# Optimization experiments

Measured on AMD Instinct MI355X. Metric: run time of the kernel, lower is better.

## Reference

```python
import jax, jax.numpy as jnp
import numpy as np

INPUT_SIZE = 256
N_DIM = 128
BATCH = 1024


def setup_inputs() -> dict:
    key = jax.random.key(0)
    ks = jax.random.split(key, 8)
    X = jax.random.normal(ks[0], (BATCH, INPUT_SIZE), dtype=jnp.float32)
    h = jax.random.normal(ks[1], (BATCH, INPUT_SIZE * N_DIM), dtype=jnp.float32)
    W_r = jax.random.normal(ks[2], (INPUT_SIZE, 1, N_DIM), dtype=jnp.float32)
    W_z = jax.random.normal(ks[3], (INPUT_SIZE, 1, N_DIM), dtype=jnp.float32)
    W_h = jax.random.normal(ks[4], (INPUT_SIZE, 1, N_DIM), dtype=jnp.float32)
    # orthogonal init for U (matches nn.init.orthogonal_ in spirit)
    def ortho(k):
        a = jax.random.normal(k, (INPUT_SIZE, N_DIM, N_DIM), dtype=jnp.float32)
        q, _ = jnp.linalg.qr(a)
        return q.astype(jnp.float32)
    U_r = ortho(ks[5])
    U_z = ortho(ks[6])
    U_h = ortho(ks[7])
    b_r = jnp.zeros((INPUT_SIZE, N_DIM), dtype=jnp.float32)
    b_z = jnp.zeros((INPUT_SIZE, N_DIM), dtype=jnp.float32)
    b_h = jnp.zeros((INPUT_SIZE, N_DIM), dtype=jnp.float32)
    return {"X": X, "h": h, "W_r": W_r, "W_z": W_z, "W_h": W_h,
            "U_r": U_r, "U_z": U_z, "U_h": U_h,
            "b_r": b_r, "b_z": b_z, "b_h": b_h}


def reference(X, h, W_r, W_z, W_h, U_r, U_z, U_h, b_r, b_z, b_h):
    B = X.shape[0]
    hg = h.reshape(B, INPUT_SIZE, N_DIM)  # [B, I, D]
    # X contribution: X[b,i] * W[i,0,k] -> [B, I, D]
    xW_r = X[:, :, None] * W_r[:, 0, :][None]
    xW_z = X[:, :, None] * W_z[:, 0, :][None]
    xW_h = X[:, :, None] * W_h[:, 0, :][None]
    # grouped GEMMs: [B,I,D] x [I,D,D] -> [B,I,D]
    r = jax.nn.sigmoid(xW_r + jnp.einsum('bij,ijk->bik', hg, U_r) + b_r)
    z = jax.nn.sigmoid(xW_z + jnp.einsum('bij,ijk->bik', hg, U_z) + b_z)
    h_tilde = jnp.tanh(xW_h + jnp.einsum('bij,ijk->bik', r * hg, U_h) + b_h)
    h_new = z * hg + (1.0 - z) * h_tilde
    return (h_new.reshape(B, INPUT_SIZE * N_DIM),
            h_tilde.reshape(B, INPUT_SIZE * N_DIM))
```

## Files before the change

### kernel.cpp

```cpp
#include <hip/hip_runtime.h>
#include <hip/hip_bf16.h>
#include <stdint.h>

#define I_SIZE 256
#define D_DIM 128
#define BATCH 1024

typedef __attribute__((ext_vector_type(8))) short short8;
typedef __attribute__((ext_vector_type(4))) short short4v;
typedef __attribute__((ext_vector_type(4))) float floatx4;

__device__ inline short f2bf(float f) {
    union { float f; uint32_t u; } v; v.f = f;
    uint32_t u = v.u;
    uint32_t r = (u + 0x7FFFu + ((u >> 16) & 1u)) >> 16;
    return (short)(r & 0xFFFFu);
}
__device__ inline float bf2f(short s) {
    union { uint32_t u; float f; } v; v.u = ((uint32_t)(uint16_t)s) << 16;
    return v.f;
}
__device__ inline uint32_t pkbf(float a, float b) {
    __hip_bfloat162 h = __float22bfloat162_rn(make_float2(a, b));
    union { __hip_bfloat162 h; uint32_t u; } v; v.h = h; return v.u;
}
__device__ inline float sigmoidf_fast(float x) { return 1.0f / (1.0f + __expf(-x)); }
__device__ inline float tanhf_fast(float x)    { return 2.0f / (1.0f + __expf(-2.0f * x)) - 1.0f; }

#define BAR_LGKM() asm volatile("s_waitcnt lgkmcnt(0)\n\ts_barrier" ::: "memory")

#define S_H 136

__global__ __launch_bounds__(1024, 4) void gru_fused(
    const float* __restrict__ X, const float* __restrict__ H,
    const float* __restrict__ Wr, const float* __restrict__ Wz, const float* __restrict__ Wh,
    const float* __restrict__ Ur, const float* __restrict__ Uz, const float* __restrict__ Uh,
    const float* __restrict__ br, const float* __restrict__ bz, const float* __restrict__ bh,
    float* __restrict__ out)
{
    __shared__ short Ut[3 * D_DIM * D_DIM];
    __shared__ short hgb[D_DIM * S_H];
    __shared__ float Wl[6][D_DIM];
    __shared__ float Xl[BATCH];

    const int tid   = threadIdx.x;
    const int group = blockIdx.x;
    const int lane  = tid & 63;
    const int w     = tid >> 6;

    if (tid < D_DIM) {
        Wl[0][tid] = Wr[group * D_DIM + tid];
        Wl[1][tid] = Wz[group * D_DIM + tid];
        Wl[2][tid] = Wh[group * D_DIM + tid];
        Wl[3][tid] = br[group * D_DIM + tid];
        Wl[4][tid] = bz[group * D_DIM + tid];
        Wl[5][tid] = bh[group * D_DIM + tid];
    }
    Xl[tid] = X[(size_t)tid * I_SIZE + group];

    {
        const int kc = tid & 127;
        const int jb = tid >> 7;
        #pragma unroll
        for (int g = 0; g < 3; ++g) {
            const float* Ug = ((g == 0) ? Ur : (g == 1) ? Uz : Uh)
                              + (size_t)group * (D_DIM * D_DIM);
            short* dst = &Ut[g * (D_DIM * D_DIM)];
            #pragma unroll
            for (int m = 0; m < 4; ++m) {
                const int j0 = m * 8 + jb;
                float a0 = Ug[(4 * j0 + 0) * D_DIM + kc];
                float a1 = Ug[(4 * j0 + 1) * D_DIM + kc];
                float a2 = Ug[(4 * j0 + 2) * D_DIM + kc];
                float a3 = Ug[(4 * j0 + 3) * D_DIM + kc];
                short4v s; s.x = f2bf(a0); s.y = f2bf(a1); s.z = f2bf(a2); s.w = f2bf(a3);
                const int p = (j0 >> 1) ^ (kc & 7);
                *(short4v*)&dst[kc * D_DIM + p * 8 + 4 * (j0 & 1)] = s;
            }
        }
    }

    const int srow = tid >> 3;
    const int scol = (tid & 7) * 4;

    #pragma unroll
    for (int it = 0; it < 4; ++it) {
        int col = scol + it * 32;
        float4 v = *(const float4*)(H + (size_t)srow * (I_SIZE * D_DIM)
                                    + group * D_DIM + col);
        uint2 uu; uu.x = pkbf(v.x, v.y); uu.y = pkbf(v.z, v.w);
        *(uint2*)&hgb[srow * S_H + col] = uu;
    }
    BAR_LGKM();

    const int am = lane & 15;
    const int aq = lane >> 4;
    const int rg = w >> 1;
    const int nh = w & 1;
    const int r0 = rg * 16;
    const size_t HOFF = (size_t)BATCH * I_SIZE * D_DIM;

    int pswz[4];
    #pragma unroll
    for (int kk = 0; kk < 4; ++kk) pswz[kk] = ((4 * kk + aq) ^ (am & 7)) * 8;

    const floatx4 zero = {0.f, 0.f, 0.f, 0.f};

    for (int pass = 0; pass < 8; ++pass) {
        const int R = pass * 128;

        short8 a[4];
        #pragma unroll
        for (int kk = 0; kk < 4; ++kk)
            a[kk] = *(const short8*)&hgb[(r0 + am) * S_H + kk * 32 + aq * 8];

        float4 pf[4];
        if (pass < 7) {
            #pragma unroll
            for (int it = 0; it < 4; ++it) {
                int col = scol + it * 32;
                pf[it] = *(const float4*)(H + (size_t)(R + 128 + srow) * (I_SIZE * D_DIM)
                                          + group * D_DIM + col);
            }
        }

        floatx4 accr[4], accz[4];
        #pragma unroll
        for (int t2 = 0; t2 < 4; ++t2) { accr[t2] = zero; accz[t2] = zero; }

        #pragma unroll
        for (int t2 = 0; t2 < 4; ++t2) {
            const int n = nh * 64 + t2 * 16 + am;
            const short* rowp = &Ut[n * D_DIM];
            #pragma unroll
            for (int kk = 0; kk < 4; ++kk)
                accr[t2] = __builtin_amdgcn_mfma_f32_16x16x32_bf16(
                    a[kk], *(const short8*)(rowp + pswz[kk]), accr[t2], 0, 0, 0);
            #pragma unroll
            for (int kk = 0; kk < 4; ++kk)
                accz[t2] = __builtin_amdgcn_mfma_f32_16x16x32_bf16(
                    a[kk], *(const short8*)(rowp + 16384 + pswz[kk]), accz[t2], 0, 0, 0);
        }

        float Xv[4];
        #pragma unroll
        for (int pp = 0; pp < 4; ++pp)
            Xv[pp] = Xl[R + r0 + aq * 4 + pp];

        float zr[4][4], hgc[4][4];
        #pragma unroll
        for (int t2 = 0; t2 < 4; ++t2) {
            const int c = nh * 64 + t2 * 16 + am;
            const float wr = Wl[0][c], wz = Wl[1][c], brv = Wl[3][c], bzv = Wl[4][c];
            #pragma unroll
            for (int pp = 0; pp < 4; ++pp) {
                const int rl = r0 + aq * 4 + pp;
                float hgv = bf2f(hgb[rl * S_H + c]);
                float rv = sigmoidf_fast(accr[t2][pp] + Xv[pp] * wr + brv);
                float zv = sigmoidf_fast(accz[t2][pp] + Xv[pp] * wz + bzv);
                zr[t2][pp]  = zv;
                hgc[t2][pp] = hgv;
                hgb[rl * S_H + c] = f2bf(rv * hgv);
            }
        }
        BAR_LGKM();

        short8 ap[4];
        #pragma unroll
        for (int kk = 0; kk < 4; ++kk)
            ap[kk] = *(const short8*)&hgb[(r0 + am) * S_H + kk * 32 + aq * 8];

        floatx4 acch[4];
        #pragma unroll
        for (int t2 = 0; t2 < 4; ++t2) acch[t2] = zero;
        #pragma unroll
        for (int t2 = 0; t2 < 4; ++t2) {
            const int n = nh * 64 + t2 * 16 + am;
            const short* rowp = &Ut[32768 + n * D_DIM];
            #pragma unroll
            for (int kk = 0; kk < 4; ++kk)
                acch[t2] = __builtin_amdgcn_mfma_f32_16x16x32_bf16(
                    ap[kk], *(const short8*)(rowp + pswz[kk]), acch[t2], 0, 0, 0);
        }

        #pragma unroll
        for (int t2 = 0; t2 < 4; ++t2) {
            const int c = nh * 64 + t2 * 16 + am;
            const float wh = Wl[2][c], bhv = Wl[5][c];
            #pragma unroll
            for (int pp = 0; pp < 4; ++pp) {
                const int rl = r0 + aq * 4 + pp;
                float ht = tanhf_fast(acch[t2][pp] + Xv[pp] * wh + bhv);
                float zv = zr[t2][pp];
                float hn = zv * hgc[t2][pp] + (1.0f - zv) * ht;
                size_t o = (size_t)(R + rl) * (I_SIZE * D_DIM) + group * D_DIM + c;
                out[o]        = hn;
                out[HOFF + o] = ht;
            }
        }

        if (pass < 7) {
            BAR_LGKM();
            #pragma unroll
            for (int it = 0; it < 4; ++it) {
                int col = scol + it * 32;
                uint2 uu; uu.x = pkbf(pf[it].x, pf[it].y); uu.y = pkbf(pf[it].z, pf[it].w);
                *(uint2*)&hgb[srow * S_H + col] = uu;
            }
            BAR_LGKM();
        }
    }
}

extern "C" void kernel_launch(void* const* d_in, const int* in_sizes, int n_in,
                              void* d_out, int out_size, void* d_ws, size_t ws_size,
                              hipStream_t stream) {
    const float* X  = (const float*)d_in[0];
    const float* H  = (const float*)d_in[1];
    const float* Wr = (const float*)d_in[2];
    const float* Wz = (const float*)d_in[3];
    const float* Wh = (const float*)d_in[4];
    const float* Ur = (const float*)d_in[5];
    const float* Uz = (const float*)d_in[6];
    const float* Uh = (const float*)d_in[7];
    const float* br = (const float*)d_in[8];
    const float* bz = (const float*)d_in[9];
    const float* bh = (const float*)d_in[10];

    (void)d_ws; (void)ws_size;

    gru_fused<<<dim3(I_SIZE), dim3(1024), 0, stream>>>(
        X, H, Wr, Wz, Wh, Ur, Uz, Uh, br, bz, bh, (float*)d_out);
}
```

Baseline: 430.7 us.

## Compute full r-gate per wave to remove mid-pass barrier, swizzle h buffer

Each wave now computes the r-gate for all 128 output columns of its 16 rows, redundantly, instead of splitting columns across a wave pair. Because each wave fills its own rows of a separate r*h buffer, the block-wide barrier between the r/z phase and the h-tilde GEMM becomes a local lgkmcnt wait. The h buffer drops its padding in favour of an XOR swizzle, W/b/X move from LDS to registers and direct global loads, and MFMA sections get s_setprio. The trade is extra r-gate MFMA and sigmoid work and more register pressure.

```diff
diff --git a/kernel.cpp b/kernel.cpp
--- a/kernel.cpp
+++ b/kernel.cpp
@@ -7,15 +7,8 @@
 #define BATCH 1024
 
 typedef __attribute__((ext_vector_type(8))) short short8;
-typedef __attribute__((ext_vector_type(4))) short short4v;
 typedef __attribute__((ext_vector_type(4))) float floatx4;
 
-__device__ inline short f2bf(float f) {
-    union { float f; uint32_t u; } v; v.f = f;
-    uint32_t u = v.u;
-    uint32_t r = (u + 0x7FFFu + ((u >> 16) & 1u)) >> 16;
-    return (short)(r & 0xFFFFu);
-}
 __device__ inline float bf2f(short s) {
     union { uint32_t u; float f; } v; v.u = ((uint32_t)(uint16_t)s) << 16;
     return v.f;
@@ -28,8 +21,6 @@
 __device__ inline float tanhf_fast(float x)    { return 2.0f / (1.0f + __expf(-2.0f * x)) - 1.0f; }
 
 #define BAR_LGKM() asm volatile("s_waitcnt lgkmcnt(0)\n\ts_barrier" ::: "memory")
-
-#define S_H 136
 
 __global__ __launch_bounds__(1024, 4) void gru_fused(
     const float* __restrict__ X, const float* __restrict__ H,
@@ -39,24 +30,36 @@
     float* __restrict__ out)
 {
     __shared__ short Ut[3 * D_DIM * D_DIM];
-    __shared__ short hgb[D_DIM * S_H];
-    __shared__ float Wl[6][D_DIM];
-    __shared__ float Xl[BATCH];
+    __shared__ short hgb[D_DIM * D_DIM];
+    __shared__ short pb [D_DIM * D_DIM];
 
     const int tid   = threadIdx.x;
     const int group = blockIdx.x;
     const int lane  = tid & 63;
     const int w     = tid >> 6;
 
-    if (tid < D_DIM) {
-        Wl[0][tid] = Wr[group * D_DIM + tid];
-        Wl[1][tid] = Wz[group * D_DIM + tid];
-        Wl[2][tid] = Wh[group * D_DIM + tid];
-        Wl[3][tid] = br[group * D_DIM + tid];
-        Wl[4][tid] = bz[group * D_DIM + tid];
-        Wl[5][tid] = bh[group * D_DIM + tid];
-    }
-    Xl[tid] = X[(size_t)tid * I_SIZE + group];
+    const int am = lane & 15;
+    const int aq = lane >> 4;
+    const int a7 = am & 7;
+    const int ah = am >> 3;
+    const int rg = w >> 1;
+    const int nh = w & 1;
+    const int r0 = rg * 16;
+    const size_t HOFF = (size_t)BATCH * I_SIZE * D_DIM;
+
+    float wrv[8], brv[8];
+    #pragma unroll
+    for (int t2 = 0; t2 < 8; ++t2) {
+        wrv[t2] = Wr[group * D_DIM + t2 * 16 + am];
+        brv[t2] = br[group * D_DIM + t2 * 16 + am];
+    }
+    float wzv[4], bzv[4], whv[4], bhv[4];
+    #pragma unroll
+    for (int t2 = 0; t2 < 4; ++t2) {
+        const int c = nh * 64 + t2 * 16 + am;
+        wzv[t2] = Wz[group * D_DIM + c]; bzv[t2] = bz[group * D_DIM + c];
+        whv[t2] = Wh[group * D_DIM + c]; bhv[t2] = bh[group * D_DIM + c];
+    }
 
     {
         const int kc = tid & 127;
@@ -73,36 +76,30 @@
                 float a1 = Ug[(4 * j0 + 1) * D_DIM + kc];
                 float a2 = Ug[(4 * j0 + 2) * D_DIM + kc];
                 float a3 = Ug[(4 * j0 + 3) * D_DIM + kc];
-                short4v s; s.x = f2bf(a0); s.y = f2bf(a1); s.z = f2bf(a2); s.w = f2bf(a3);
+                uint2 uu; uu.x = pkbf(a0, a1); uu.y = pkbf(a2, a3);
                 const int p = (j0 >> 1) ^ (kc & 7);
-                *(short4v*)&dst[kc * D_DIM + p * 8 + 4 * (j0 & 1)] = s;
+                *(uint2*)&dst[kc * D_DIM + p * 8 + 4 * (j0 & 1)] = uu;
             }
         }
     }
 
     const int srow = tid >> 3;
-    const int scol = (tid & 7) * 4;
+    const int sblk = (tid & 7) >> 1;
+    const int sof  = (tid & 7 & 1) * 4;
+    const int sr7  = (srow & 7) << 3;
 
     #pragma unroll
     for (int it = 0; it < 4; ++it) {
-        int col = scol + it * 32;
         float4 v = *(const float4*)(H + (size_t)srow * (I_SIZE * D_DIM)
-                                    + group * D_DIM + col);
+                                    + group * D_DIM + (tid & 7) * 4 + it * 32);
         uint2 uu; uu.x = pkbf(v.x, v.y); uu.y = pkbf(v.z, v.w);
-        *(uint2*)&hgb[srow * S_H + col] = uu;
+        *(uint2*)&hgb[(srow << 7) + ((((sblk + it * 4) << 3) ^ sr7)) + sof] = uu;
     }
     BAR_LGKM();
 
-    const int am = lane & 15;
-    const int aq = lane >> 4;
-    const int rg = w >> 1;
-    const int nh = w & 1;
-    const int r0 = rg * 16;
-    const size_t HOFF = (size_t)BATCH * I_SIZE * D_DIM;
-
     int pswz[4];
     #pragma unroll
-    for (int kk = 0; kk < 4; ++kk) pswz[kk] = ((4 * kk + aq) ^ (am & 7)) * 8;
+    for (int kk = 0; kk < 4; ++kk) pswz[kk] = (((4 * kk + aq) << 3) ^ (a7 << 3));
 
     const floatx4 zero = {0.f, 0.f, 0.f, 0.f};
 
@@ -112,88 +109,103 @@
         short8 a[4];
         #pragma unroll
         for (int kk = 0; kk < 4; ++kk)
-            a[kk] = *(const short8*)&hgb[(r0 + am) * S_H + kk * 32 + aq * 8];
+            a[kk] = *(const short8*)&hgb[((r0 + am) << 7) + pswz[kk]];
+
+        float Xv[4];
+        #pragma unroll
+        for (int pp = 0; pp < 4; ++pp)
+            Xv[pp] = X[(size_t)(R + r0 + aq * 4 + pp) * I_SIZE + group];
 
         float4 pf[4];
         if (pass < 7) {
             #pragma unroll
-            for (int it = 0; it < 4; ++it) {
-                int col = scol + it * 32;
+            for (int it = 0; it < 4; ++it)
                 pf[it] = *(const float4*)(H + (size_t)(R + 128 + srow) * (I_SIZE * D_DIM)
-                                          + group * D_DIM + col);
-            }
-        }
-
-        floatx4 accr[4], accz[4];
-        #pragma unroll
-        for (int t2 = 0; t2 < 4; ++t2) { accr[t2] = zero; accz[t2] = zero; }
-
-        #pragma unroll
-        for (int t2 = 0; t2 < 4; ++t2) {
-            const int n = nh * 64 + t2 * 16 + am;
-            const short* rowp = &Ut[n * D_DIM];
+                                          + group * D_DIM + (tid & 7) * 4 + it * 32);
+        }
+
+        floatx4 accr[8];
+        #pragma unroll
+        for (int t2 = 0; t2 < 8; ++t2) accr[t2] = zero;
+        __builtin_amdgcn_s_setprio(1);
+        #pragma unroll
+        for (int t2 = 0; t2 < 8; ++t2) {
+            const short* rowp = &Ut[(t2 * 16 + am) << 7];
             #pragma unroll
             for (int kk = 0; kk < 4; ++kk)
                 accr[t2] = __builtin_amdgcn_mfma_f32_16x16x32_bf16(
                     a[kk], *(const short8*)(rowp + pswz[kk]), accr[t2], 0, 0, 0);
+        }
+        __builtin_amdgcn_s_setprio(0);
+
+        #pragma unroll
+        for (int pp = 0; pp < 4; ++pp) {
+            const int rl = r0 + aq * 4 + pp;
+            const int rb = rl << 7;
+            const int rx = (rl & 7) << 3;
+            float pv[8];
+            #pragma unroll
+            for (int t2 = 0; t2 < 8; ++t2) {
+                const float hgv = bf2f(hgb[rb + ((((t2 * 2 + ah) << 3) ^ rx)) + a7]);
+                const float rv  = sigmoidf_fast(accr[t2][pp] + Xv[pp] * wrv[t2] + brv[t2]);
+                pv[t2] = rv * hgv;
+            }
+            #pragma unroll
+            for (int te = 0; te < 4; ++te) {
+                const uint32_t u = pkbf(pv[2 * te], pv[2 * te + 1]);
+                pb[rb + ((((4 * te + ah) << 3) ^ rx)) + a7]     = (short)(u & 0xFFFFu);
+                pb[rb + ((((4 * te + 2 + ah) << 3) ^ rx)) + a7] = (short)(u >> 16);
+            }
+        }
+
+        floatx4 accz[4];
+        #pragma unroll
+        for (int t2 = 0; t2 < 4; ++t2) accz[t2] = zero;
+        __builtin_amdgcn_s_setprio(1);
+        #pragma unroll
+        for (int t2 = 0; t2 < 4; ++t2) {
+            const short* rowp = &Ut[16384 + ((nh * 64 + t2 * 16 + am) << 7)];
             #pragma unroll
             for (int kk = 0; kk < 4; ++kk)
                 accz[t2] = __builtin_amdgcn_mfma_f32_16x16x32_bf16(
-                    a[kk], *(const short8*)(rowp + 16384 + pswz[kk]), accz[t2], 0, 0, 0);
-        }
-
-        float Xv[4];
-        #pragma unroll
-        for (int pp = 0; pp < 4; ++pp)
-            Xv[pp] = Xl[R + r0 + aq * 4 + pp];
-
-        float zr[4][4], hgc[4][4];
+                    a[kk], *(const short8*)(rowp + pswz[kk]), accz[t2], 0, 0, 0);
+        }
+        __builtin_amdgcn_s_setprio(0);
+
+        asm volatile("s_waitcnt lgkmcnt(0)" ::: "memory");
+        __builtin_amdgcn_sched_barrier(0);
+
+        short8 ap[4];
+        #pragma unroll
+        for (int kk = 0; kk < 4; ++kk)
+            ap[kk] = *(const short8*)&pb[((r0 + am) << 7) + pswz[kk]];
+
+        floatx4 acch[4];
+        #pragma unroll
+        for (int t2 = 0; t2 < 4; ++t2) acch[t2] = zero;
+        __builtin_amdgcn_s_setprio(1);
         #pragma unroll
         for (int t2 = 0; t2 < 4; ++t2) {
-            const int c = nh * 64 + t2 * 16 + am;
-            const float wr = Wl[0][c], wz = Wl[1][c], brv = Wl[3][c], bzv = Wl[4][c];
-            #pragma unroll
-            for (int pp = 0; pp < 4; ++pp) {
-                const int rl = r0 + aq * 4 + pp;
-                float hgv = bf2f(hgb[rl * S_H + c]);
-                float rv = sigmoidf_fast(accr[t2][pp] + Xv[pp] * wr + brv);
-                float zv = sigmoidf_fast(accz[t2][pp] + Xv[pp] * wz + bzv);
-                zr[t2][pp]  = zv;
-                hgc[t2][pp] = hgv;
-                hgb[rl * S_H + c] = f2bf(rv * hgv);
-            }
-        }
-        BAR_LGKM();
-
-        short8 ap[4];
-        #pragma unroll
-        for (int kk = 0; kk < 4; ++kk)
-            ap[kk] = *(const short8*)&hgb[(r0 + am) * S_H + kk * 32 + aq * 8];
-
-        floatx4 acch[4];
-        #pragma unroll
-        for (int t2 = 0; t2 < 4; ++t2) acch[t2] = zero;
-        #pragma unroll
-        for (int t2 = 0; t2 < 4; ++t2) {
-            const int n = nh * 64 + t2 * 16 + am;
-            const short* rowp = &Ut[32768 + n * D_DIM];
+            const short* rowp = &Ut[32768 + ((nh * 64 + t2 * 16 + am) << 7)];
             #pragma unroll
             for (int kk = 0; kk < 4; ++kk)
                 acch[t2] = __builtin_amdgcn_mfma_f32_16x16x32_bf16(
                     ap[kk], *(const short8*)(rowp + pswz[kk]), acch[t2], 0, 0, 0);
         }
+        __builtin_amdgcn_s_setprio(0);
 
         #pragma unroll
         for (int t2 = 0; t2 < 4; ++t2) {
-            const int c = nh * 64 + t2 * 16 + am;
-            const float wh = Wl[2][c], bhv = Wl[5][c];
+            const int c  = nh * 64 + t2 * 16 + am;
+            const int cb = (nh * 8 + t2 * 2 + ah) << 3;
             #pragma unroll
             for (int pp = 0; pp < 4; ++pp) {
                 const int rl = r0 + aq * 4 + pp;
-                float ht = tanhf_fast(acch[t2][pp] + Xv[pp] * wh + bhv);
-                float zv = zr[t2][pp];
-                float hn = zv * hgc[t2][pp] + (1.0f - zv) * ht;
-                size_t o = (size_t)(R + rl) * (I_SIZE * D_DIM) + group * D_DIM + c;
+                const float hgv = bf2f(hgb[(rl << 7) + (cb ^ ((rl & 7) << 3)) + a7]);
+                const float zv = sigmoidf_fast(accz[t2][pp] + Xv[pp] * wzv[t2] + bzv[t2]);
+                const float ht = tanhf_fast(acch[t2][pp] + Xv[pp] * whv[t2] + bhv[t2]);
+                const float hn = zv * hgv + (1.0f - zv) * ht;
+                const size_t o = (size_t)(R + rl) * (I_SIZE * D_DIM) + group * D_DIM + c;
                 out[o]        = hn;
                 out[HOFF + o] = ht;
             }
@@ -203,9 +215,8 @@
             BAR_LGKM();
             #pragma unroll
             for (int it = 0; it < 4; ++it) {
-                int col = scol + it * 32;
                 uint2 uu; uu.x = pkbf(pf[it].x, pf[it].y); uu.y = pkbf(pf[it].z, pf[it].w);
-                *(uint2*)&hgb[srow * S_H + col] = uu;
+                *(uint2*)&hgb[(srow << 7) + ((((sblk + it * 4) << 3) ^ sr7)) + sof] = uu;
             }
             BAR_LGKM();
         }
```

After: 673.1 us. +56.3%, slower.
